# Optimization experiments

Measured on AMD Instinct MI355X. Metric: run time of the kernel, lower is better.

Reference implementation:

```python
import jax, jax.numpy as jnp
import numpy as np
import math

N = 100000          # total nodes across all subgraphs
E = 1600000         # directed edges (avg degree 16)
H = 128             # hidden_channels
MAXZ = 1000         # max_z
G = 1000            # number of subgraphs (unique batch ids)
NPG = N // G        # nodes per subgraph
L = 3               # num_layers


def setup_inputs() -> dict:
    key = jax.random.key(0)
    ks = jax.random.split(key, 9)
    z = jax.random.randint(ks[0], (N,), 0, MAXZ, dtype=jnp.int32)
    edge_index = jax.random.randint(ks[1], (2, E), 0, N, dtype=jnp.int32)
    batch = jnp.repeat(jnp.arange(G, dtype=jnp.int32), NPG)  # sorted graph ids
    s = 1.0 / math.sqrt(H)
    z_emb_table = jax.random.normal(ks[2], (MAXZ, H), jnp.float32) * 0.1
    conv_w = jax.random.normal(ks[3], (L, H, H), jnp.float32) * s
    conv_b = jnp.zeros((L, H), jnp.float32)
    mlp_w1 = jax.random.normal(ks[4], (H, H), jnp.float32) * s
    mlp_b1 = jnp.zeros((H,), jnp.float32)
    mlp_w2 = jax.random.normal(ks[5], (H, 1), jnp.float32) * s
    mlp_b2 = jnp.zeros((1,), jnp.float32)
    return {"num_nodes": N, "z": z, "edge_index": edge_index, "batch": batch,
            "z_emb_table": z_emb_table, "conv_w": conv_w, "conv_b": conv_b,
            "mlp_w1": mlp_w1, "mlp_b1": mlp_b1, "mlp_w2": mlp_w2, "mlp_b2": mlp_b2}


def reference(num_nodes, z, edge_index, batch, z_emb_table, conv_w, conv_b,
              mlp_w1, mlp_b1, mlp_w2, mlp_b2):
    # --- GCN normalization (PyG GCNConv: add self-loops, sym deg norm) ---
    loops = jnp.arange(num_nodes, dtype=edge_index.dtype)
    src = jnp.concatenate([edge_index[0], loops])  # [E+N]
    dst = jnp.concatenate([edge_index[1], loops])
    deg = jax.ops.segment_sum(jnp.ones_like(dst, jnp.float32), dst,
                              num_segments=num_nodes)
    dinv = jnp.where(deg > 0, jax.lax.rsqrt(deg), 0.0)
    norm = (dinv[src] * dinv[dst])[:, None]        # [E+N, 1]

    # --- embedding lookup (eval mode: no dropedge/dropout) ---
    x = z_emb_table[z]                             # [N, H]

    # --- stacked GCNConv: linear -> gather -> normalize -> scatter-add ---
    for l in range(L):
        h = x @ conv_w[l]                          # [N, H]
        h = jax.ops.segment_sum(h[src] * norm, dst, num_segments=num_nodes)
        h = h + conv_b[l]
        x = jax.nn.relu(h) if l < L - 1 else h

    # --- center-node pooling: first occurrence of each batch id ---
    first = jnp.concatenate([jnp.array([True]), batch[1:] != batch[:-1]])
    ci = jnp.nonzero(first, size=G)[0]             # [G]
    xs = x[ci] * x[ci + 1]                         # src * dst node features

    # --- MLP head [H, H, 1] (batch_norm=False, eval: dropout off) ---
    h = jax.nn.relu(xs @ mlp_w1 + mlp_b1)
    return h @ mlp_w2 + mlp_b2                     # [G, 1]
```

## Files before the change

kernel.cpp:

```cpp
#include <hip/hip_runtime.h>
#include <hip/hip_fp16.h>

#define HD 128
#define BSH 9
#define NBLKA 256
#define CAP 96
#define EDSCAP 10240
#define CAPB 12288
#define RPAD 136

typedef _Float16 half8_t __attribute__((ext_vector_type(8)));
typedef float floatx4 __attribute__((ext_vector_type(4)));

__device__ inline unsigned pack_h2(float x, float y) {
  __half2 h = __floats2half2_rn(x, y);
  return __builtin_bit_cast(unsigned, h);
}
__device__ inline float2 up_h2(unsigned u) {
  __half2 h = __builtin_bit_cast(__half2, u);
  return __half22float2(h);
}

__device__ inline void add8(float* acc, uint4 r) {
  float2 f;
  f = up_h2(r.x); acc[0] += f.x; acc[1] += f.y;
  f = up_h2(r.y); acc[2] += f.x; acc[3] += f.y;
  f = up_h2(r.z); acc[4] += f.x; acc[5] += f.y;
  f = up_h2(r.w); acc[6] += f.x; acc[7] += f.y;
}

__global__ __launch_bounds__(256) void k_phase0(const int* __restrict__ src,
                                                const int* __restrict__ dst, int E, int nbuck,
                                                unsigned* __restrict__ bpool,
                                                int* __restrict__ counts,
                                                const float* __restrict__ conv_w,
                                                uint4* __restrict__ wfrag,
                                                const int* __restrict__ batch,
                                                int* __restrict__ ci,
                                                int* __restrict__ flag,
                                                int n) {
  __shared__ int cnt[512];
  int b = blockIdx.x;
  if (b < NBLKA) {
    for (int i = threadIdx.x; i < nbuck; i += 256) cnt[i] = 0;
    __syncthreads();
    int chunk = (E + NBLKA - 1) / NBLKA;
    int lo = b * chunk, hi = min(E, lo + chunk);
    for (int i = lo + threadIdx.x; i < hi; i += 256) {
      int s = src[i], d = dst[i];
      int bk = d >> BSH;
      int c = atomicAdd(&cnt[bk], 1);
      if (c < CAP)
        bpool[((size_t)bk * NBLKA + b) * CAP + c] =
            ((unsigned)(d & ((1 << BSH) - 1)) << 23) | (unsigned)s;
    }
    __syncthreads();
    for (int bk = threadIdx.x; bk < nbuck; bk += 256) counts[(size_t)bk * NBLKA + b] = cnt[bk];
  } else if (b < NBLKA + 24) {
    int t = (b - NBLKA) * 256 + threadIdx.x;
    int lane = t & 63;
    int s = (t >> 6) & 3;
    int c4 = (t >> 8) & 3;
    int chalf = (t >> 10) & 1;
    int layer = t >> 11;
    int col = chalf * 64 + c4 * 16 + (lane & 15);
    int k0 = s * 32 + (lane >> 4) * 8;
    const float* W = conv_w + (size_t)layer * HD * HD;
    unsigned u[4];
#pragma unroll
    for (int j = 0; j < 4; ++j)
      u[j] = pack_h2(W[(size_t)(k0 + 2 * j) * HD + col], W[(size_t)(k0 + 2 * j + 1) * HD + col]);
    uint4 o; o.x = u[0]; o.y = u[1]; o.z = u[2]; o.w = u[3];
    wfrag[t] = o;
  } else {
    int i = (b - NBLKA - 24) * 256 + threadIdx.x;
    if (i >= n) return;
    flag[i] = 0;
    if (i == 0) flag[n] = 0;
    if (i == 0 || batch[i] != batch[i - 1]) ci[batch[i]] = i;
  }
}

__global__ __launch_bounds__(256) void k_build(const unsigned* __restrict__ bpool,
                                               const int* __restrict__ counts,
                                               int n, float* __restrict__ dinv,
                                               int* __restrict__ rowstart,
                                               int* __restrict__ rowend,
                                               int* __restrict__ col) {
  __shared__ unsigned eds[EDSCAP];
  __shared__ int hist[1 << BSH];
  __shared__ int wsum[256];
  __shared__ int coff[NBLKA + 1];
  int b = blockIdx.x;
  int t = threadIdx.x;
  int v = (t < NBLKA) ? min(counts[(size_t)b * NBLKA + t], CAP) : 0;
  wsum[t] = v;
  __syncthreads();
  for (int off = 1; off < NBLKA; off <<= 1) {
    int x = (t >= off) ? wsum[t - off] : 0;
    __syncthreads();
    wsum[t] += x;
    __syncthreads();
  }
  if (t < NBLKA) coff[t] = wsum[t] - v;
  if (t == NBLKA - 1) coff[NBLKA] = wsum[NBLKA - 1];
  __syncthreads();
  int total = min(coff[NBLKA], EDSCAP);
  int w = t >> 6, lane = t & 63;
  for (int blk = w; blk < NBLKA; blk += 4) {
    int off0 = coff[blk], len = coff[blk + 1] - off0;
    const unsigned* seg = bpool + ((size_t)b * NBLKA + blk) * CAP;
    for (int i = lane; i < len; i += 64)
      if (off0 + i < EDSCAP) eds[off0 + i] = seg[i];
  }
  for (int i = t; i < (1 << BSH); i += 256) hist[i] = 0;
  __syncthreads();
  for (int i = t; i < total; i += 256) atomicAdd(&hist[eds[i] >> 23], 1);
  __syncthreads();
  int base = b << BSH;
  int nn = min(1 << BSH, n - base);
  int a0 = hist[2 * t], a1 = hist[2 * t + 1];
  int s = a0 + a1;
  wsum[t] = s;
  __syncthreads();
  for (int off = 1; off < 256; off <<= 1) {
    int x = (t >= off) ? wsum[t - off] : 0;
    __syncthreads();
    wsum[t] += x;
    __syncthreads();
  }
  int excl = wsum[t] - s;
  int cbase = b * CAPB;
  if (2 * t < nn) {
    rowstart[base + 2 * t] = cbase + excl;
    rowend[base + 2 * t] = cbase + excl + a0;
    dinv[base + 2 * t] = 1.0f / sqrtf((float)(a0 + 1));
  }
  if (2 * t + 1 < nn) {
    rowstart[base + 2 * t + 1] = cbase + excl + a0;
    rowend[base + 2 * t + 1] = cbase + excl + s;
    dinv[base + 2 * t + 1] = 1.0f / sqrtf((float)(a1 + 1));
  }
  hist[2 * t] = cbase + excl;
  hist[2 * t + 1] = cbase + excl + a0;
  __syncthreads();
  for (int i = t; i < total; i += 256) {
    unsigned pk = eds[i];
    int dl = pk >> 23;
    int pos = atomicAdd(&hist[dl], 1);
    col[pos] = (int)(pk & 0x7FFFFF);
  }
}

__global__ __launch_bounds__(64) void k_active(const int* __restrict__ ci,
                                               const int* __restrict__ rowstart,
                                               const int* __restrict__ rowend,
                                               const int* __restrict__ col,
                                               int g2, int* __restrict__ flag,
                                               int* __restrict__ list, int n) {
  int lane = threadIdx.x;
  int vid = blockIdx.x * 64 + lane;
  bool haveRow = vid < g2;
  int* nactive = flag + n;
  int node = 0, e = 0, end = 0;
  if (haveRow) {
    node = ci[vid >> 1] + (vid & 1);
    e = rowstart[node];
    end = rowend[node];
  }
  bool neu = haveRow && (atomicExch(&flag[node], 1) == 0);
  unsigned long long m = __ballot(neu);
  int base = 0;
  if (lane == 0 && m) base = atomicAdd(nactive, __popcll(m));
  base = __shfl(base, 0);
  if (neu) list[base + __popcll(m & ((1ULL << lane) - 1))] = node;
  for (;;) {
    bool act = haveRow && (e < end);
    if (!__any(act)) break;
    int s = act ? col[e] : 0;
    bool nw = act && (atomicExch(&flag[s], 1) == 0);
    unsigned long long mm = __ballot(nw);
    int b2 = 0;
    if (lane == 0 && mm) b2 = atomicAdd(nactive, __popcll(mm));
    b2 = __shfl(b2, 0);
    if (nw) list[b2 + __popcll(mm & ((1ULL << lane) - 1))] = s;
    ++e;
  }
}

__device__ inline void gemm16(const _Float16* xs, const uint4* __restrict__ wfragL,
                              const float* __restrict__ dinv, uint2* __restrict__ Yh,
                              int row0, int nvalid, const int* __restrict__ rowmap,
                              int tid) {
  int lane = tid & 63, w = tid >> 6;
  int chalf = w >> 1, h = lane >> 4;
  half8_t wf[8];
#pragma unroll
  for (int cc = 0; cc < 2; ++cc)
#pragma unroll
    for (int s = 0; s < 4; ++s) {
      int c4 = 2 * (w & 1) + cc;
      wf[cc * 4 + s] = __builtin_bit_cast(half8_t,
          wfragL[((chalf * 4 + c4) * 4 + s) * 64 + lane]);
    }
  half8_t bf[4];
#pragma unroll
  for (int s = 0; s < 4; ++s)
    bf[s] = *(const half8_t*)&xs[(size_t)(lane & 15) * RPAD + (s * 4 + h) * 8];
  floatx4 acc[2];
  acc[0] = (floatx4){0.f, 0.f, 0.f, 0.f};
  acc[1] = (floatx4){0.f, 0.f, 0.f, 0.f};
#pragma unroll
  for (int s = 0; s < 4; ++s) {
    acc[0] = __builtin_amdgcn_mfma_f32_16x16x32_f16(wf[s], bf[s], acc[0], 0, 0, 0);
    acc[1] = __builtin_amdgcn_mfma_f32_16x16x32_f16(wf[4 + s], bf[s], acc[1], 0, 0, 0);
  }
  int i = row0 + (lane & 15);
  if (i < nvalid) {
    int orow = rowmap ? rowmap[i] : i;
    float dv = dinv[orow];
#pragma unroll
    for (int cc = 0; cc < 2; ++cc) {
      int c4 = 2 * (w & 1) + cc;
      int colbase = chalf * 64 + c4 * 16 + h * 4;
      uint2 o;
      o.x = pack_h2(acc[cc][0] * dv, acc[cc][1] * dv);
      o.y = pack_h2(acc[cc][2] * dv, acc[cc][3] * dv);
      Yh[(size_t)orow * 32 + (colbase >> 2)] = o;
    }
  }
}

__global__ __launch_bounds__(256) void k_embgemm(const int* __restrict__ z,
                                                 const float4* __restrict__ emb,
                                                 const uint4* __restrict__ wfragL,
                                                 const float* __restrict__ dinv,
                                                 uint2* __restrict__ Yh, int n) {
  __shared__ __align__(16) _Float16 xs[16 * RPAD];
  int tid = threadIdx.x;
  int grp = tid >> 4, li = tid & 15;
  int node = blockIdx.x * 16 + grp;
  int nd = node < n ? node : n - 1;
  const float4* er = emb + (size_t)z[nd] * 32 + li * 2;
  float4 f0 = er[0], f1 = er[1];
  uint4 hx;
  hx.x = pack_h2(f0.x, f0.y); hx.y = pack_h2(f0.z, f0.w);
  hx.z = pack_h2(f1.x, f1.y); hx.w = pack_h2(f1.z, f1.w);
  *(uint4*)&xs[(size_t)grp * RPAD + li * 8] = hx;
  __syncthreads();
  gemm16(xs, wfragL, dinv, Yh, blockIdx.x * 16, n, nullptr, tid);
}

__global__ __launch_bounds__(256) void k_agg_gemm(const uint4* __restrict__ H,
                                                  const int* __restrict__ rowstart,
                                                  const int* __restrict__ rowend,
                                                  const int* __restrict__ col,
                                                  const float* __restrict__ dinv,
                                                  const float* __restrict__ bias,
                                                  const uint4* __restrict__ wfragL,
                                                  uint2* __restrict__ Yh, int n) {
  __shared__ __align__(16) _Float16 xs[16 * RPAD];
  int tid = threadIdx.x;
  int grp = tid >> 4, li = tid & 15;
  int node = blockIdx.x * 16 + grp;
  int nd = node < n ? node : n - 1;
  uint4 srow = H[(size_t)nd * 16 + li];
  float acc[8] = {0.f, 0.f, 0.f, 0.f, 0.f, 0.f, 0.f, 0.f};
  add8(acc, srow);
  int e = rowstart[nd], end = rowend[nd];
  for (; e + 3 < end; e += 4) {
    int c0 = col[e], c1 = col[e + 1], c2 = col[e + 2], c3 = col[e + 3];
    uint4 r0 = H[(size_t)c0 * 16 + li];
    uint4 r1 = H[(size_t)c1 * 16 + li];
    uint4 r2 = H[(size_t)c2 * 16 + li];
    uint4 r3 = H[(size_t)c3 * 16 + li];
    add8(acc, r0);
    add8(acc, r1);
    add8(acc, r2);
    add8(acc, r3);
  }
  for (; e < end; ++e) {
    uint4 r = H[(size_t)col[e] * 16 + li];
    add8(acc, r);
  }
  float dv = dinv[nd];
  float4 b0 = ((const float4*)bias)[2 * li];
  float4 b1 = ((const float4*)bias)[2 * li + 1];
  acc[0] = fmaxf(fmaf(dv, acc[0], b0.x), 0.f);
  acc[1] = fmaxf(fmaf(dv, acc[1], b0.y), 0.f);
  acc[2] = fmaxf(fmaf(dv, acc[2], b0.z), 0.f);
  acc[3] = fmaxf(fmaf(dv, acc[3], b0.w), 0.f);
  acc[4] = fmaxf(fmaf(dv, acc[4], b1.x), 0.f);
  acc[5] = fmaxf(fmaf(dv, acc[5], b1.y), 0.f);
  acc[6] = fmaxf(fmaf(dv, acc[6], b1.z), 0.f);
  acc[7] = fmaxf(fmaf(dv, acc[7], b1.w), 0.f);
  uint4 hx;
  hx.x = pack_h2(acc[0], acc[1]); hx.y = pack_h2(acc[2], acc[3]);
  hx.z = pack_h2(acc[4], acc[5]); hx.w = pack_h2(acc[6], acc[7]);
  *(uint4*)&xs[(size_t)grp * RPAD + li * 8] = hx;
  __syncthreads();
  gemm16(xs, wfragL, dinv, Yh, blockIdx.x * 16, n, nullptr, tid);
}

__global__ __launch_bounds__(256) void k_agg_gemmL(const uint4* __restrict__ H,
                                                   const int* __restrict__ rowstart,
                                                   const int* __restrict__ rowend,
                                                   const int* __restrict__ col,
                                                   const float* __restrict__ dinv,
                                                   const float* __restrict__ bias,
                                                   const uint4* __restrict__ wfragL,
                                                   uint2* __restrict__ Yh,
                                                   const int* __restrict__ list,
                                                   const int* __restrict__ nactive) {
  __shared__ __align__(16) _Float16 xs[16 * RPAD];
  int na = *nactive;
  int tid = threadIdx.x;
  int grp = tid >> 4, li = tid & 15;
  for (int tile = blockIdx.x; tile * 16 < na; tile += gridDim.x) {
    int i = tile * 16 + grp;
    int node = list[i < na ? i : na - 1];
    uint4 srow = H[(size_t)node * 16 + li];
    float acc[8] = {0.f, 0.f, 0.f, 0.f, 0.f, 0.f, 0.f, 0.f};
    add8(acc, srow);
    int e = rowstart[node], end = rowend[node];
    for (; e + 3 < end; e += 4) {
      int c0 = col[e], c1 = col[e + 1], c2 = col[e + 2], c3 = col[e + 3];
      uint4 r0 = H[(size_t)c0 * 16 + li];
      uint4 r1 = H[(size_t)c1 * 16 + li];
      uint4 r2 = H[(size_t)c2 * 16 + li];
      uint4 r3 = H[(size_t)c3 * 16 + li];
      add8(acc, r0);
      add8(acc, r1);
      add8(acc, r2);
      add8(acc, r3);
    }
    for (; e < end; ++e) {
      uint4 r = H[(size_t)col[e] * 16 + li];
      add8(acc, r);
    }
    float dv = dinv[node];
    float4 b0 = ((const float4*)bias)[2 * li];
    float4 b1 = ((const float4*)bias)[2 * li + 1];
    acc[0] = fmaxf(fmaf(dv, acc[0], b0.x), 0.f);
    acc[1] = fmaxf(fmaf(dv, acc[1], b0.y), 0.f);
    acc[2] = fmaxf(fmaf(dv, acc[2], b0.z), 0.f);
    acc[3] = fmaxf(fmaf(dv, acc[3], b0.w), 0.f);
    acc[4] = fmaxf(fmaf(dv, acc[4], b1.x), 0.f);
    acc[5] = fmaxf(fmaf(dv, acc[5], b1.y), 0.f);
    acc[6] = fmaxf(fmaf(dv, acc[6], b1.z), 0.f);
    acc[7] = fmaxf(fmaf(dv, acc[7], b1.w), 0.f);
    uint4 hx;
    hx.x = pack_h2(acc[0], acc[1]); hx.y = pack_h2(acc[2], acc[3]);
    hx.z = pack_h2(acc[4], acc[5]); hx.w = pack_h2(acc[6], acc[7]);
    *(uint4*)&xs[(size_t)grp * RPAD + li * 8] = hx;
    __syncthreads();
    gemm16(xs, wfragL, dinv, Yh, tile * 16, na, list, tid);
    __syncthreads();
  }
}

__global__ __launch_bounds__(256) void k_aggF(const uint4* __restrict__ H,
                                              const int* __restrict__ rowstart,
                                              const int* __restrict__ rowend,
                                              const int* __restrict__ col,
                                              const float* __restrict__ dinv,
                                              const float* __restrict__ bias,
                                              const int* __restrict__ ci,
                                              uint4* __restrict__ Xc, int g2) {
  int li = threadIdx.x & 15;
  int vid = blockIdx.x * 16 + (threadIdx.x >> 4);
  if (vid >= g2) return;
  int node = ci[vid >> 1] + (vid & 1);
  uint4 srow = H[(size_t)node * 16 + li];
  float acc[8] = {0.f, 0.f, 0.f, 0.f, 0.f, 0.f, 0.f, 0.f};
  add8(acc, srow);
  int e = rowstart[node], end = rowend[node];
  for (; e + 3 < end; e += 4) {
    int c0 = col[e], c1 = col[e + 1], c2 = col[e + 2], c3 = col[e + 3];
    uint4 r0 = H[(size_t)c0 * 16 + li];
    uint4 r1 = H[(size_t)c1 * 16 + li];
    uint4 r2 = H[(size_t)c2 * 16 + li];
    uint4 r3 = H[(size_t)c3 * 16 + li];
    add8(acc, r0);
    add8(acc, r1);
    add8(acc, r2);
    add8(acc, r3);
  }
  for (; e < end; ++e) {
    uint4 r = H[(size_t)col[e] * 16 + li];
    add8(acc, r);
  }
  float dv = dinv[node];
  float4 b0 = ((const float4*)bias)[2 * li];
  float4 b1 = ((const float4*)bias)[2 * li + 1];
  acc[0] = fmaf(dv, acc[0], b0.x); acc[1] = fmaf(dv, acc[1], b0.y);
  acc[2] = fmaf(dv, acc[2], b0.z); acc[3] = fmaf(dv, acc[3], b0.w);
  acc[4] = fmaf(dv, acc[4], b1.x); acc[5] = fmaf(dv, acc[5], b1.y);
  acc[6] = fmaf(dv, acc[6], b1.z); acc[7] = fmaf(dv, acc[7], b1.w);
  uint4 o;
  o.x = pack_h2(acc[0], acc[1]);
  o.y = pack_h2(acc[2], acc[3]);
  o.z = pack_h2(acc[4], acc[5]);
  o.w = pack_h2(acc[6], acc[7]);
  Xc[(size_t)vid * 16 + li] = o;
}

__global__ __launch_bounds__(128) void k_head(const __half* __restrict__ Xc,
                                              const float* __restrict__ W1,
                                              const float* __restrict__ b1,
                                              const float* __restrict__ w2,
                                              const float* __restrict__ b2,
                                              float* __restrict__ out, int G) {
  __shared__ float xs[HD];
  __shared__ float red[HD];
  int g = blockIdx.x;
  int t = threadIdx.x;
  xs[t] = __half2float(Xc[(size_t)(2 * g) * HD + t]) *
          __half2float(Xc[(size_t)(2 * g + 1) * HD + t]);
  __syncthreads();
  float acc = b1[t];
#pragma unroll 8
  for (int k = 0; k < HD; ++k) acc = fmaf(xs[k], W1[k * HD + t], acc);
  acc = fmaxf(acc, 0.f);
  red[t] = acc * w2[t];
  __syncthreads();
  for (int off = 64; off > 0; off >>= 1) {
    if (t < off) red[t] += red[t + off];
    __syncthreads();
  }
  if (t == 0) out[g] = red[0] + b2[0];
}

extern "C" void kernel_launch(void* const* d_in, const int* in_sizes, int n_in,
                              void* d_out, int out_size, void* d_ws, size_t ws_size,
                              hipStream_t stream) {
  (void)n_in; (void)ws_size;
  const int*   z      = (const int*)d_in[1];
  const int*   ei     = (const int*)d_in[2];
  const int*   batch  = (const int*)d_in[3];
  const float* emb    = (const float*)d_in[4];
  const float* conv_w = (const float*)d_in[5];
  const float* conv_b = (const float*)d_in[6];
  const float* w1     = (const float*)d_in[7];
  const float* b1     = (const float*)d_in[8];
  const float* w2     = (const float*)d_in[9];
  const float* b2     = (const float*)d_in[10];
  int n = in_sizes[1];
  int E = in_sizes[2] / 2;
  int G = out_size;
  const int* esrc = ei;
  const int* edst = ei + E;
  int nbuck = (n + (1 << BSH) - 1) >> BSH;

  char* p = (char*)d_ws;
  auto alloc = [&](size_t bytes) { void* r = (void*)p; p += (bytes + 255) / 256 * 256; return r; };
  unsigned* bufA     = (unsigned*)alloc((size_t)n * HD * 2);
  unsigned* bufB     = (unsigned*)alloc((size_t)n * HD * 2);
  unsigned* bufC     = (unsigned*)alloc((size_t)2 * G * HD * 2);
  float*    dinv     = (float*)alloc((size_t)n * 4);
  int*      rowstart = (int*)alloc((size_t)n * 4);
  int*      rowend   = (int*)alloc((size_t)n * 4);
  int*      col      = (int*)alloc((size_t)nbuck * CAPB * 4);
  uint4*    wfrag    = (uint4*)alloc((size_t)3 * 2048 * 16);
  int*      ci       = (int*)alloc((size_t)G * 4);
  int*      flag     = (int*)alloc((size_t)(n + 64) * 4);
  int*      list     = (int*)alloc((size_t)n * 4);
  unsigned* bpool    = (unsigned*)alloc((size_t)nbuck * NBLKA * CAP * 4);
  int*      counts   = (int*)alloc((size_t)nbuck * NBLKA * 4);

  int ciBlocks = (n + 255) / 256;
  int g2 = 2 * G;
  int* nactive = flag + n;

  k_phase0<<<NBLKA + 24 + ciBlocks, 256, 0, stream>>>(
      esrc, edst, E, nbuck, bpool, counts, conv_w, wfrag, batch, ci, flag, n);
  k_build<<<nbuck, 256, 0, stream>>>(bpool, counts, n, dinv, rowstart, rowend, col);
  k_embgemm<<<(n + 15) / 16, 256, 0, stream>>>(z, (const float4*)emb, wfrag, dinv,
                                               (uint2*)bufB, n);
  k_active<<<(g2 + 63) / 64, 64, 0, stream>>>(ci, rowstart, rowend, col, g2, flag, list, n);
  k_agg_gemm<<<(n + 15) / 16, 256, 0, stream>>>((const uint4*)bufB, rowstart, rowend, col,
                                                dinv, conv_b, wfrag + 2048, (uint2*)bufA, n);
  k_agg_gemmL<<<512, 256, 0, stream>>>((const uint4*)bufA, rowstart, rowend, col, dinv,
                                       conv_b + HD, wfrag + 4096, (uint2*)bufB, list, nactive);
  k_aggF<<<(g2 + 15) / 16, 256, 0, stream>>>((const uint4*)bufB, rowstart, rowend, col, dinv,
                                             conv_b + 2 * HD, ci, (uint4*)bufC, g2);
  k_head<<<G, 128, 0, stream>>>((const __half*)bufC, w1, b1, w2, b2, (float*)d_out, G);
}
```

Baseline: 232.3 us.

## Swizzle shared-memory tile layout and fuse final aggregation into MLP head kernel

Replaces the padded shared-memory row layout with an XOR swizzle so the tile needs no padding while still avoiding LDS bank conflicts. Merges the last-layer aggregation for center-node pairs into the head kernel, removing one launch and the intermediate buffer. Each head block splits a node's edge list across four thread groups and reduces their partial sums in shared memory. The final aggregation now stays in fp32 instead of being rounded to fp16, which slightly changes numerics.

```diff
diff --git a/kernel.cpp b/kernel.cpp
--- a/kernel.cpp
+++ b/kernel.cpp
@@ -7,7 +7,7 @@
 #define CAP 96
 #define EDSCAP 10240
 #define CAPB 12288
-#define RPAD 136
+#define XSW(row, c8) (((size_t)(row) << 7) + ((size_t)(((c8) ^ ((row) & 7))) << 3))
 
 typedef _Float16 half8_t __attribute__((ext_vector_type(8)));
 typedef float floatx4 __attribute__((ext_vector_type(4)));
@@ -206,7 +206,7 @@
   half8_t bf[4];
 #pragma unroll
   for (int s = 0; s < 4; ++s)
-    bf[s] = *(const half8_t*)&xs[(size_t)(lane & 15) * RPAD + (s * 4 + h) * 8];
+    bf[s] = *(const half8_t*)&xs[XSW(lane & 15, s * 4 + h)];
   floatx4 acc[2];
   acc[0] = (floatx4){0.f, 0.f, 0.f, 0.f};
   acc[1] = (floatx4){0.f, 0.f, 0.f, 0.f};
@@ -236,7 +236,7 @@
                                                  const uint4* __restrict__ wfragL,
                                                  const float* __restrict__ dinv,
                                                  uint2* __restrict__ Yh, int n) {
-  __shared__ __align__(16) _Float16 xs[16 * RPAD];
+  __shared__ __align__(16) _Float16 xs[16 * HD];
   int tid = threadIdx.x;
   int grp = tid >> 4, li = tid & 15;
   int node = blockIdx.x * 16 + grp;
@@ -246,7 +246,7 @@
   uint4 hx;
   hx.x = pack_h2(f0.x, f0.y); hx.y = pack_h2(f0.z, f0.w);
   hx.z = pack_h2(f1.x, f1.y); hx.w = pack_h2(f1.z, f1.w);
-  *(uint4*)&xs[(size_t)grp * RPAD + li * 8] = hx;
+  *(uint4*)&xs[XSW(grp, li)] = hx;
   __syncthreads();
   gemm16(xs, wfragL, dinv, Yh, blockIdx.x * 16, n, nullptr, tid);
 }
@@ -259,7 +259,7 @@
                                                   const float* __restrict__ bias,
                                                   const uint4* __restrict__ wfragL,
                                                   uint2* __restrict__ Yh, int n) {
-  __shared__ __align__(16) _Float16 xs[16 * RPAD];
+  __shared__ __align__(16) _Float16 xs[16 * HD];
   int tid = threadIdx.x;
   int grp = tid >> 4, li = tid & 15;
   int node = blockIdx.x * 16 + grp;
@@ -297,7 +297,7 @@
   uint4 hx;
   hx.x = pack_h2(acc[0], acc[1]); hx.y = pack_h2(acc[2], acc[3]);
   hx.z = pack_h2(acc[4], acc[5]); hx.w = pack_h2(acc[6], acc[7]);
-  *(uint4*)&xs[(size_t)grp * RPAD + li * 8] = hx;
+  *(uint4*)&xs[XSW(grp, li)] = hx;
   __syncthreads();
   gemm16(xs, wfragL, dinv, Yh, blockIdx.x * 16, n, nullptr, tid);
 }
@@ -312,7 +312,7 @@
                                                    uint2* __restrict__ Yh,
                                                    const int* __restrict__ list,
                                                    const int* __restrict__ nactive) {
-  __shared__ __align__(16) _Float16 xs[16 * RPAD];
+  __shared__ __align__(16) _Float16 xs[16 * HD];
   int na = *nactive;
   int tid = threadIdx.x;
   int grp = tid >> 4, li = tid & 15;
@@ -352,77 +352,55 @@
     uint4 hx;
     hx.x = pack_h2(acc[0], acc[1]); hx.y = pack_h2(acc[2], acc[3]);
     hx.z = pack_h2(acc[4], acc[5]); hx.w = pack_h2(acc[6], acc[7]);
-    *(uint4*)&xs[(size_t)grp * RPAD + li * 8] = hx;
+    *(uint4*)&xs[XSW(grp, li)] = hx;
     __syncthreads();
     gemm16(xs, wfragL, dinv, Yh, tile * 16, na, list, tid);
     __syncthreads();
   }
 }
 
-__global__ __launch_bounds__(256) void k_aggF(const uint4* __restrict__ H,
+__global__ __launch_bounds__(128) void k_tail(const uint4* __restrict__ H,
                                               const int* __restrict__ rowstart,
                                               const int* __restrict__ rowend,
                                               const int* __restrict__ col,
                                               const float* __restrict__ dinv,
                                               const float* __restrict__ bias,
                                               const int* __restrict__ ci,
-                                              uint4* __restrict__ Xc, int g2) {
-  int li = threadIdx.x & 15;
-  int vid = blockIdx.x * 16 + (threadIdx.x >> 4);
-  if (vid >= g2) return;
-  int node = ci[vid >> 1] + (vid & 1);
-  uint4 srow = H[(size_t)node * 16 + li];
-  float acc[8] = {0.f, 0.f, 0.f, 0.f, 0.f, 0.f, 0.f, 0.f};
-  add8(acc, srow);
-  int e = rowstart[node], end = rowend[node];
-  for (; e + 3 < end; e += 4) {
-    int c0 = col[e], c1 = col[e + 1], c2 = col[e + 2], c3 = col[e + 3];
-    uint4 r0 = H[(size_t)c0 * 16 + li];
-    uint4 r1 = H[(size_t)c1 * 16 + li];
-    uint4 r2 = H[(size_t)c2 * 16 + li];
-    uint4 r3 = H[(size_t)c3 * 16 + li];
-    add8(acc, r0);
-    add8(acc, r1);
-    add8(acc, r2);
-    add8(acc, r3);
-  }
-  for (; e < end; ++e) {
-    uint4 r = H[(size_t)col[e] * 16 + li];
-    add8(acc, r);
-  }
-  float dv = dinv[node];
-  float4 b0 = ((const float4*)bias)[2 * li];
-  float4 b1 = ((const float4*)bias)[2 * li + 1];
-  acc[0] = fmaf(dv, acc[0], b0.x); acc[1] = fmaf(dv, acc[1], b0.y);
-  acc[2] = fmaf(dv, acc[2], b0.z); acc[3] = fmaf(dv, acc[3], b0.w);
-  acc[4] = fmaf(dv, acc[4], b1.x); acc[5] = fmaf(dv, acc[5], b1.y);
-  acc[6] = fmaf(dv, acc[6], b1.z); acc[7] = fmaf(dv, acc[7], b1.w);
-  uint4 o;
-  o.x = pack_h2(acc[0], acc[1]);
-  o.y = pack_h2(acc[2], acc[3]);
-  o.z = pack_h2(acc[4], acc[5]);
-  o.w = pack_h2(acc[6], acc[7]);
-  Xc[(size_t)vid * 16 + li] = o;
-}
-
-__global__ __launch_bounds__(128) void k_head(const __half* __restrict__ Xc,
                                               const float* __restrict__ W1,
                                               const float* __restrict__ b1,
                                               const float* __restrict__ w2,
                                               const float* __restrict__ b2,
                                               float* __restrict__ out, int G) {
+  __shared__ float part[8][HD];
   __shared__ float xs[HD];
   __shared__ float red[HD];
   int g = blockIdx.x;
   int t = threadIdx.x;
-  xs[t] = __half2float(Xc[(size_t)(2 * g) * HD + t]) *
-          __half2float(Xc[(size_t)(2 * g + 1) * HD + t]);
-  __syncthreads();
-  float acc = b1[t];
+  int grp = t >> 4, li = t & 15;
+  int nodeA = ci[g];
+  int node = nodeA + (grp >> 2);
+  int gi = grp & 3;
+  float acc[8] = {0.f, 0.f, 0.f, 0.f, 0.f, 0.f, 0.f, 0.f};
+  if (gi == 0) add8(acc, H[(size_t)node * 16 + li]);
+  for (int e = rowstart[node] + gi; e < rowend[node]; e += 4) {
+    uint4 r = H[(size_t)col[e] * 16 + li];
+    add8(acc, r);
+  }
+#pragma unroll
+  for (int j = 0; j < 8; ++j) part[grp][li * 8 + j] = acc[j];
+  __syncthreads();
+  float sumA = part[0][t] + part[1][t] + part[2][t] + part[3][t];
+  float sumB = part[4][t] + part[5][t] + part[6][t] + part[7][t];
+  float bb = bias[t];
+  float va = fmaf(dinv[nodeA], sumA, bb);
+  float vb = fmaf(dinv[nodeA + 1], sumB, bb);
+  xs[t] = va * vb;
+  __syncthreads();
+  float hacc = b1[t];
 #pragma unroll 8
-  for (int k = 0; k < HD; ++k) acc = fmaf(xs[k], W1[k * HD + t], acc);
-  acc = fmaxf(acc, 0.f);
-  red[t] = acc * w2[t];
+  for (int k = 0; k < HD; ++k) hacc = fmaf(xs[k], W1[k * HD + t], hacc);
+  hacc = fmaxf(hacc, 0.f);
+  red[t] = hacc * w2[t];
   __syncthreads();
   for (int off = 64; off > 0; off >>= 1) {
     if (t < off) red[t] += red[t + off];
@@ -456,7 +434,6 @@
   auto alloc = [&](size_t bytes) { void* r = (void*)p; p += (bytes + 255) / 256 * 256; return r; };
   unsigned* bufA     = (unsigned*)alloc((size_t)n * HD * 2);
   unsigned* bufB     = (unsigned*)alloc((size_t)n * HD * 2);
-  unsigned* bufC     = (unsigned*)alloc((size_t)2 * G * HD * 2);
   float*    dinv     = (float*)alloc((size_t)n * 4);
   int*      rowstart = (int*)alloc((size_t)n * 4);
   int*      rowend   = (int*)alloc((size_t)n * 4);
@@ -482,7 +459,6 @@
                                                 dinv, conv_b, wfrag + 2048, (uint2*)bufA, n);
   k_agg_gemmL<<<512, 256, 0, stream>>>((const uint4*)bufA, rowstart, rowend, col, dinv,
                                        conv_b + HD, wfrag + 4096, (uint2*)bufB, list, nactive);
-  k_aggF<<<(g2 + 15) / 16, 256, 0, stream>>>((const uint4*)bufB, rowstart, rowend, col, dinv,
-                                             conv_b + 2 * HD, ci, (uint4*)bufC, g2);
-  k_head<<<G, 128, 0, stream>>>((const __half*)bufC, w1, b1, w2, b2, (float*)d_out, G);
-}
+  k_tail<<<G, 128, 0, stream>>>((const uint4*)bufB, rowstart, rowend, col, dinv,
+                                conv_b + 2 * HD, ci, w1, b1, w2, b2, (float*)d_out, G);
+}
```

Result: faster. 226.8 us (-2.4%).
